# Optimization experiments

Measured on AMD Instinct MI355X. Metric: run time of the kernel, lower is better.

The kernel has to match this reference:

```python
import jax, jax.numpy as jnp
import numpy as np

H_IMG, W_IMG = 60, 80          # hardcoded grid in get_positional_encodings
NUM_HEADS = 8
DIM = 256
N_TOK = H_IMG * W_IMG          # 4800

# Hardcoded intrinsics in the source: fx=517/9, fy=517/8, cx=40, cy=30.
# fx_norm = fx/(2*cx)*2, fy_norm = fy/(2*cy)*2 ; cx_norm = cy_norm = 0,
# so Kinv is diagonal and Kinv @ [x, y, 1] = [x/fx_n, y/fy_n, 1].
_FX_N = (517.0 / 9.0) / 80.0 * 2.0
_FY_N = (517.0 / 8.0) / 60.0 * 2.0


def _positional(B):
    ys = jnp.linspace(-1.0, 1.0, H_IMG)
    xs = jnp.linspace(-1.0, 1.0, W_IMG)
    # loop index j*w + k: y varies over rows (outer), x over cols (inner)
    p3 = jnp.repeat(ys, W_IMG) / _FY_N   # (N,) = y'/w'
    p4 = jnp.tile(xs, H_IMG) / _FX_N     # (N,) = x'/w'
    pos = jnp.stack([p3 * p3, p4 * p4, p3 * p4, p3, p4, jnp.ones_like(p3)], axis=-1)  # (N,6)
    return jnp.broadcast_to(pos, (B, N_TOK, 6))


def setup_inputs() -> dict:
    key = jax.random.key(0)
    k1, k2, k3, k4, k5 = jax.random.split(key, 5)
    B, N, C, H = 1, N_TOK, DIM, NUM_HEADS
    return {
        "x1": jax.random.normal(k1, (B, N, C), dtype=jnp.float32),
        "x2": jax.random.normal(k2, (B, N, C), dtype=jnp.float32),
        "qkv_w": jax.random.normal(k3, (3 * C, C), dtype=jnp.float32) * 0.02,
        "proj_w": jax.random.normal(k4, (C, C + 6 * H), dtype=jnp.float32) * 0.02,
        "proj_b": jax.random.normal(k5, (C,), dtype=jnp.float32) * 0.02,
    }


def reference(x1, x2, qkv_w, proj_w, proj_b):
    B, N, C = x1.shape
    H = NUM_HEADS
    hd = C // H
    scale = hd ** -0.5
    D = hd + 6

    def qkv(x):
        y = (x @ qkv_w.T).reshape(B, N, 3, H, hd).transpose(2, 0, 3, 1, 4)
        return y[0], y[1], y[2]   # each (B,H,N,hd)

    q1, k1, v1 = qkv(x1)
    q2, k2, v2 = qkv(x2)

    pos_h = jnp.broadcast_to(_positional(B)[:, None], (B, H, N, 6))

    def fundamental(q, k, v):
        a = jnp.einsum('bhnd,bhmd->bhnm', q, k) * scale          # (B,H,N,N)
        af = jax.nn.softmax(a, axis=-1) * jax.nn.softmax(a, axis=-2)  # dual softmax
        vc = jnp.concatenate([v, pos_h], axis=-1)                 # (B,H,N,D)
        f = jnp.einsum('bhnc,bhnm->bhcm', vc, af)                 # V^T A
        f = jnp.einsum('bhcm,bhmd->bhcd', f, vc)                  # (V^T A) V -> (B,H,D,D)
        f = f.reshape(B, H * D, D).transpose(0, 2, 1)             # (B, D, H*D)
        return f @ proj_w.T + proj_b                              # (B, D, C)

    fundamental_1 = fundamental(q2, k1, v1)
    fundamental_2 = fundamental(q1, k2, v2)
    return fundamental_2, fundamental_1
```

## Files before the change

### kernel.cpp

```cpp
#include <hip/hip_runtime.h>
#include <stdint.h>
#include <math.h>

#define N_TOK 4800
#define NH 8
#define HD 32
#define DP 40
#define DD 38
#define NTILES 150
#define MCHUNK 3
#define FRAG 2048
#define SCALE 0.17677669529663687f
#define QSCALE (0.17677669529663687f * 1.4426950408889634f)

typedef float f32x16 __attribute__((ext_vector_type(16)));
typedef short s8v __attribute__((ext_vector_type(8)));
typedef int i2v __attribute__((ext_vector_type(2)));

#if __has_builtin(__builtin_amdgcn_exp2f)
#define EXP2F(x) __builtin_amdgcn_exp2f(x)
#else
#define EXP2F(x) exp2f(x)
#endif

__device__ __forceinline__ unsigned short f2bf(float x) {
    union { float f; uint32_t u; } v; v.f = x;
    uint32_t r = v.u + 0x7FFFu + ((v.u >> 16) & 1u);
    return (unsigned short)(r >> 16);
}
__device__ __forceinline__ float bf2f(unsigned short h) {
    union { uint32_t u; float f; } v; v.u = ((uint32_t)h) << 16;
    return v.f;
}
__device__ __forceinline__ int cvtpk(float lo, float hi) {
    int r;
    asm("v_cvt_pk_bf16_f32 %0, %1, %2" : "=v"(r) : "v"(lo), "v"(hi));
    return r;
}
__device__ __forceinline__ s8v mk_s8(int a, int b, int c, int d) {
    union { int i[4]; s8v s; } u;
    u.i[0] = a; u.i[1] = b; u.i[2] = c; u.i[3] = d;
    return u.s;
}

template<int NX, int NY>
__device__ __forceinline__ void swzdec(int& x, int& y, int& z) {
    const int L = blockIdx.x + NX * (blockIdx.y + NY * blockIdx.z);
    constexpr int cpx = NX * NY * 16 / 8;
    const int s = (L & 7) * cpx + (L >> 3);
    x = s % NX;
    const int r = s / NX;
    y = r % NY;
    z = r / NY;
}

#define MFMA(a, b, c) __builtin_amdgcn_mfma_f32_32x32x16_bf16((a), (b), (c), 0, 0, 0)

__global__ __launch_bounds__(256) void frag_kernel(
    const float* __restrict__ x1, unsigned short* __restrict__ xh1,
    unsigned short* __restrict__ xl1,
    const float* __restrict__ x2, unsigned short* __restrict__ xh2,
    unsigned short* __restrict__ xl2,
    const float* __restrict__ w, unsigned short* __restrict__ wh,
    unsigned short* __restrict__ wl)
{
    int b = blockIdx.x;
    const float* src; unsigned short* dh; unsigned short* dl;
    if (b < 150)      { src = x1 + b * 8192; dh = xh1 + b * 8192; dl = xl1 + b * 8192; }
    else if (b < 300) { b -= 150; src = x2 + b * 8192; dh = xh2 + b * 8192; dl = xl2 + b * 8192; }
    else              { b -= 300; src = w + b * 8192; dh = wh + b * 8192; dl = wl + b * 8192; }
    const int t = threadIdx.x;
#pragma unroll
    for (int k = 0; k < 4; ++k) {
        const int f = k * 256 + t;
        const int c = f >> 6;
        const int rem = f & 63;
        const int hi5 = rem >> 5, lr = rem & 31;
        const float* sp = src + lr * 256 + c * 16 + hi5 * 8;
        const float4 a = *(const float4*)(sp);
        const float4 bb = *(const float4*)(sp + 4);
        const float vv[8] = {a.x, a.y, a.z, a.w, bb.x, bb.y, bb.z, bb.w};
        union { unsigned short s[8]; s8v v; } H, L;
#pragma unroll
        for (int j = 0; j < 8; ++j) {
            H.s[j] = f2bf(vv[j]);
            L.s[j] = f2bf(vv[j] - bf2f(H.s[j]));
        }
        *(s8v*)(dh + f * 8) = H.v;
        *(s8v*)(dl + f * 8) = L.v;
    }
}

__global__ __launch_bounds__(128) void qkv_mfma_kernel(
    const unsigned short* __restrict__ xhA, const unsigned short* __restrict__ xlA,
    unsigned short* __restrict__ qbA, unsigned short* __restrict__ kbA,
    float* __restrict__ vcbA,
    const unsigned short* __restrict__ xhB, const unsigned short* __restrict__ xlB,
    unsigned short* __restrict__ qbB, unsigned short* __restrict__ kbB,
    float* __restrict__ vcbB,
    const unsigned short* __restrict__ wh, const unsigned short* __restrict__ wl)
{
    const int sel = blockIdx.z;
    const unsigned short* xh = sel ? xhB : xhA;
    const unsigned short* xl = sel ? xlB : xlA;
    unsigned short* qb = sel ? qbB : qbA;
    unsigned short* kb = sel ? kbB : kbA;
    float* vcb = sel ? vcbB : vcbA;
    const int lane = threadIdx.x & 63;
    const int wid = threadIdx.x >> 6;
    const int xtile = blockIdx.x * 2 + wid;
    const int n0 = xtile * 32;
    const int j0 = blockIdx.y * 32;
    const int lr = lane & 31, hi5 = lane >> 5;
    const unsigned short* xhp = xh + (size_t)xtile * 8192 + lane * 8;
    const unsigned short* xlp = xl + (size_t)xtile * 8192 + lane * 8;
    const unsigned short* whp = wh + (size_t)blockIdx.y * 8192 + lane * 8;
    const unsigned short* wlp = wl + (size_t)blockIdx.y * 8192 + lane * 8;
    f32x16 acc = {};
#pragma unroll 4
    for (int c = 0; c < 16; ++c) {
        const s8v aH = *(const s8v*)(xhp + c * 512);
        const s8v aL = *(const s8v*)(xlp + c * 512);
        const s8v bH = *(const s8v*)(whp + c * 512);
        const s8v bL = *(const s8v*)(wlp + c * 512);
        acc = MFMA(aH, bH, acc);
        acc = MFMA(aH, bL, acc);
        acc = MFMA(aL, bH, acc);
    }
    const int s = j0 >> 8, h = (j0 >> 5) & 7, d = lr;
#pragma unroll
    for (int r = 0; r < 16; ++r) {
        const int n = n0 + (r & 3) + 8 * (r >> 2) + 4 * hi5;
        const float v = acc[r];
        if (s == 2)      vcb[(h * N_TOK + n) * DP + d] = v;
        else if (s == 0) qb[(h * N_TOK + n) * HD + d] = f2bf(v * QSCALE);
        else             kb[(h * N_TOK + n) * HD + d] = f2bf(v);
    }
}

__global__ void pos_kernel(float* __restrict__ vc1, float* __restrict__ vc2)
{
    const int n = blockIdx.x * 256 + threadIdx.x;
    if (n >= N_TOK) return;
    const int row = n / 80, col = n % 80;
    const float y = -1.0f + 2.0f * (float)row / 59.0f;
    const float x = -1.0f + 2.0f * (float)col / 79.0f;
    const float p3 = y * (240.0f / 517.0f);
    const float p4 = x * (360.0f / 517.0f);
    const float pv[8] = {p3 * p3, p4 * p4, p3 * p4, p3, p4, 1.0f, 0.0f, 0.0f};
#pragma unroll
    for (int h = 0; h < NH; ++h) {
        const size_t base = (size_t)(h * N_TOK + n) * DP + 32;
#pragma unroll
        for (int p = 0; p < 8; ++p) {
            vc1[base + p] = pv[p];
            vc2[base + p] = pv[p];
        }
    }
}

__global__ __launch_bounds__(128) void cs_kernel(
    const unsigned short* __restrict__ qbA, const unsigned short* __restrict__ kbA,
    float* __restrict__ csA,
    const unsigned short* __restrict__ qbB, const unsigned short* __restrict__ kbB,
    float* __restrict__ csB)
{
    int bx, by, bz;
    swzdec<75, 5>(bx, by, bz);
    const int sel = bz >> 3;
    const unsigned short* qb = sel ? qbB : qbA;
    const unsigned short* kb = sel ? kbB : kbA;
    float* cs = sel ? csB : csA;
    const int lane = threadIdx.x & 63;
    const int wid = threadIdx.x >> 6;
    const int h = bz & 7;
    const int m0 = bx * 64 + wid * 32;
    const int lr = lane & 31, hi5 = lane >> 5;
    const int hbase = h * N_TOK;
    const unsigned short* kp = kb + (hbase + m0 + lr) * HD + 8 * hi5;
    const s8v bK0 = *(const s8v*)(kp);
    const s8v bK1 = *(const s8v*)(kp + 16);
    const int nt0 = by * 30;
    const unsigned short* qp = qb + (hbase + nt0 * 32 + lr) * HD + 8 * hi5;
    s8v a0 = *(const s8v*)(qp);
    s8v a1 = *(const s8v*)(qp + 16);
    float csa = 0.f, csb = 0.f;
#pragma unroll 2
    for (int it = 0; it < 30; ++it) {
        const int adv = (it < 29) ? (32 * HD) : 0;
        const unsigned short* qpn = qp + adv;
        const s8v na0 = *(const s8v*)(qpn);
        const s8v na1 = *(const s8v*)(qpn + 16);
        f32x16 acc = {};
        acc = MFMA(a0, bK0, acc);
        acc = MFMA(a1, bK1, acc);
#pragma unroll
        for (int r = 0; r < 16; r += 2) {
            csa += EXP2F(acc[r]);
            csb += EXP2F(acc[r + 1]);
        }
        a0 = na0; a1 = na1; qp = qpn;
    }
    float csacc = csa + csb;
    csacc += __shfl_xor(csacc, 32);
    if (lane < 32) atomicAdd(&cs[hbase + m0 + lane], csacc);
}

__global__ __launch_bounds__(256) void vfrag_kernel(
    const float* __restrict__ vcA, const float* __restrict__ csA,
    unsigned short* __restrict__ vfA,
    const float* __restrict__ vcB, const float* __restrict__ csB,
    unsigned short* __restrict__ vfB)
{
    const int sel = blockIdx.y >> 3;
    const float* vc = sel ? vcB : vcA;
    const float* cs = sel ? csB : csA;
    unsigned short* vf = sel ? vfB : vfA;
    __shared__ float vl[32][41];
    __shared__ float ul[32];
    const int mt = blockIdx.x;
    const int h = blockIdx.y & 7;
    const int t = threadIdx.x;
    const int m0 = mt * 32;
    const float* vcbase = vc + (size_t)(h * N_TOK + m0) * DP;
    for (int e = t; e < 32 * DP; e += 256) vl[e / DP][e % DP] = vcbase[e];
    if (t < 32) ul[t] = 1.0f / cs[(size_t)h * N_TOK + m0 + t];
    __syncthreads();
    const int b = t >> 6, lane = t & 63;
    const int hi5 = lane >> 5, lr = lane & 31;
    const int d = (b >> 1) * 32 + lr;
    const int mb = (b & 1) * 16 + hi5 * 8;
    union { unsigned short s[8]; s8v v; } pk;
#pragma unroll
    for (int j = 0; j < 8; ++j) {
        const int mo = mb + j;
        const float v = (d < DP) ? vl[mo][d] * ul[mo] : 0.0f;
        pk.s[j] = f2bf(v);
    }
    *(s8v*)(vf + ((size_t)(h * NTILES + mt) * 4 + b) * 512 + lane * 8) = pk.v;
}

__global__ __launch_bounds__(128, 3) void tprime_mfma_kernel(
    const unsigned short* __restrict__ qbA, const unsigned short* __restrict__ kbA,
    const unsigned short* __restrict__ vfA, float* __restrict__ rsA,
    float* __restrict__ TA0, float* __restrict__ TA1, float* __restrict__ TA2,
    const unsigned short* __restrict__ qbB, const unsigned short* __restrict__ kbB,
    const unsigned short* __restrict__ vfB, float* __restrict__ rsB,
    float* __restrict__ TB0, float* __restrict__ TB1, float* __restrict__ TB2)
{
    int bx, by, bz;
    swzdec<75, MCHUNK>(bx, by, bz);
    const int sel = bz >> 3;
    const unsigned short* qb = sel ? qbB : qbA;
    const unsigned short* kb = sel ? kbB : kbA;
    const unsigned short* vf = sel ? vfB : vfA;
    float* rs = sel ? rsB : rsA;
    float* T = sel ? (by == 0 ? TB0 : (by == 1 ? TB1 : TB2))
                   : (by == 0 ? TA0 : (by == 1 ? TA1 : TA2));
    const int lane = threadIdx.x & 63;
    const int wid = threadIdx.x >> 6;
    const int h = bz & 7;
    const int n0 = bx * 64 + wid * 32;
    const int lr = lane & 31, hi5 = lane >> 5;
    const int hbase = h * N_TOK;
    const unsigned short* qp = qb + (hbase + n0 + lr) * HD + 8 * hi5;
    const s8v bQ0 = *(const s8v*)(qp);
    const s8v bQ1 = *(const s8v*)(qp + 16);
    f32x16 t0 = {}, t1 = {};
    float rsa = 0.f, rsb = 0.f;
    const int mt0 = by * 50;
    const unsigned short* kp = kb + (hbase + mt0 * 32 + lr) * HD + 8 * hi5;
    const unsigned short* vp = vf + ((size_t)(h * NTILES) + mt0) * FRAG + lane * 8;
    s8v a0 = *(const s8v*)(kp);
    s8v a1 = *(const s8v*)(kp + 16);
    s8v v00 = *(const s8v*)(vp);
    s8v v01 = *(const s8v*)(vp + 512);
    s8v v10 = *(const s8v*)(vp + 1024);
    s8v v11 = *(const s8v*)(vp + 1536);
#pragma unroll 2
    for (int it = 0; it < 50; ++it) {
        const int adv = (it < 49) ? 1 : 0;
        const unsigned short* kpn = kp + adv * 32 * HD;
        const unsigned short* vpn = vp + adv * FRAG;
        const s8v na0 = *(const s8v*)(kpn);
        const s8v na1 = *(const s8v*)(kpn + 16);
        const s8v nv00 = *(const s8v*)(vpn);
        const s8v nv01 = *(const s8v*)(vpn + 512);
        const s8v nv10 = *(const s8v*)(vpn + 1024);
        const s8v nv11 = *(const s8v*)(vpn + 1536);
        f32x16 s = {};
        s = MFMA(a0, bQ0, s);
        s = MFMA(a1, bQ1, s);
        float p[16];
#pragma unroll
        for (int r = 0; r < 16; r += 2) {
            const float e0 = EXP2F(s[r]);
            const float e1 = EXP2F(s[r + 1]);
            rsa += e0; rsb += e1;
            p[r] = e0 * e0; p[r + 1] = e1 * e1;
        }
        const int L0 = cvtpk(p[0], p[1]),   L1 = cvtpk(p[2], p[3]);
        const int H0 = cvtpk(p[4], p[5]),   H1 = cvtpk(p[6], p[7]);
        const int L2 = cvtpk(p[8], p[9]),   L3 = cvtpk(p[10], p[11]);
        const int H2 = cvtpk(p[12], p[13]), H3 = cvtpk(p[14], p[15]);
        const i2v s0 = __builtin_amdgcn_permlane32_swap(L0, H0, false, false);
        const i2v s1 = __builtin_amdgcn_permlane32_swap(L1, H1, false, false);
        const i2v s2 = __builtin_amdgcn_permlane32_swap(L2, H2, false, false);
        const i2v s3 = __builtin_amdgcn_permlane32_swap(L3, H3, false, false);
        const s8v pa0 = mk_s8(s0[0], s1[0], s0[1], s1[1]);
        const s8v pa1 = mk_s8(s2[0], s3[0], s2[1], s3[1]);
        __builtin_amdgcn_s_setprio(1);
        t0 = MFMA(pa0, v00, t0);
        t0 = MFMA(pa1, v01, t0);
        t1 = MFMA(pa0, v10, t1);
        t1 = MFMA(pa1, v11, t1);
        __builtin_amdgcn_s_setprio(0);
        a0 = na0; a1 = na1; kp = kpn;
        v00 = nv00; v01 = nv01; v10 = nv10; v11 = nv11; vp = vpn;
    }
    float rsacc = rsa + rsb;
    rsacc += __shfl_xor(rsacc, 32);
    if (lane < 32) atomicAdd(&rs[hbase + n0 + lane], rsacc);
#pragma unroll
    for (int r = 0; r < 16; ++r) {
        const int n = n0 + (r & 3) + 8 * (r >> 2) + 4 * hi5;
        T[(size_t)(hbase + n) * DP + lr] = t0[r];
    }
    if (lr < 8) {
#pragma unroll
        for (int r = 0; r < 16; ++r) {
            const int n = n0 + (r & 3) + 8 * (r >> 2) + 4 * hi5;
            T[(size_t)(hbase + n) * DP + 32 + lr] = t1[r];
        }
    }
}

__global__ __launch_bounds__(256) void fgemm_kernel(
    const float* __restrict__ VCA, const float* __restrict__ rsA,
    const float* __restrict__ TA0, const float* __restrict__ TA1,
    const float* __restrict__ TA2, float* __restrict__ fA,
    const float* __restrict__ VCB, const float* __restrict__ rsB,
    const float* __restrict__ TB0, const float* __restrict__ TB1,
    const float* __restrict__ TB2, float* __restrict__ fB)
{
    const int sel = blockIdx.x >> 3;
    const float* VC = sel ? VCB : VCA;
    const float* rs = sel ? rsB : rsA;
    const float* Ta = sel ? TB0 : TA0;
    const float* Tb = sel ? TB1 : TA1;
    const float* Tc = sel ? TB2 : TA2;
    float* f = sel ? fB : fA;
    __shared__ __align__(16) float wvcl[64 * DP];
    __shared__ __align__(16) float tl[64 * DP];
    __shared__ float wl[64];
    const int h = blockIdx.x & 7, n0 = blockIdx.y * 64;
    const int t = threadIdx.x;
    if (t < 64) wl[t] = 1.0f / rs[(size_t)h * N_TOK + n0 + t];
    __syncthreads();
    const float* vcbase = VC + (size_t)(h * N_TOK + n0) * DP;
    const float* tabase = Ta + (size_t)(h * N_TOK + n0) * DP;
    const float* tbbase = Tb + (size_t)(h * N_TOK + n0) * DP;
    const float* tcbase = Tc + (size_t)(h * N_TOK + n0) * DP;
    for (int e = t; e < 64 * DP; e += 256) {
        wvcl[e] = vcbase[e] * wl[e / DP];
        tl[e] = tabase[e] + tbbase[e] + tcbase[e];
    }
    __syncthreads();
    for (int p = t; p < DD * DD; p += 256) {
        const int c = p / DD, d = p % DD;
        float s = 0.f;
#pragma unroll 8
        for (int n = 0; n < 64; ++n) s += wvcl[n * DP + c] * tl[n * DP + d];
        atomicAdd(&f[(size_t)(h * DD + c) * DP + d], s);
    }
}

__global__ __launch_bounds__(256) void out_kernel(
    const float* __restrict__ f1, const float* __restrict__ f2,
    const float* __restrict__ pw, const float* __restrict__ pb,
    float* __restrict__ out)
{
    const int sel = blockIdx.y;
    const float* f = sel ? f2 : f1;
    float* dst = sel ? out : (out + DD * 256);
    __shared__ __align__(16) float flds[304];
    const int d = blockIdx.x, t = threadIdx.x;
    for (int j = t; j < 304; j += 256) flds[j] = f[(size_t)j * DP + d];
    __syncthreads();
    float acc = pb[t];
    const float* pwrow = pw + (size_t)t * 304;
#pragma unroll 4
    for (int j = 0; j < 304; j += 4) {
        const float4 p4 = *(const float4*)&pwrow[j];
        const float4 f4 = *(const float4*)&flds[j];
        acc += p4.x * f4.x + p4.y * f4.y + p4.z * f4.z + p4.w * f4.w;
    }
    dst[(size_t)d * 256 + t] = acc;
}

extern "C" void kernel_launch(void* const* d_in, const int* in_sizes, int n_in,
                              void* d_out, int out_size, void* d_ws, size_t ws_size,
                              hipStream_t stream)
{
    const float* x1 = (const float*)d_in[0];
    const float* x2 = (const float*)d_in[1];
    const float* qkv_w = (const float*)d_in[2];
    const float* proj_w = (const float*)d_in[3];
    const float* proj_b = (const float*)d_in[4];
    float* out = (float*)d_out;

    const size_t QSZ = (size_t)NH * N_TOK * HD;
    const size_t VSZ = (size_t)NH * N_TOK * DP;
    const size_t SSZ = (size_t)NH * N_TOK;
    const size_t FSZ = (size_t)NH * DD * DP;
    const size_t XSZ = (size_t)N_TOK * 256;
    const size_t WSZ = (size_t)768 * 256;
    const size_t VTSZ = (size_t)NH * NTILES * FRAG;

    float* vc1 = (float*)d_ws;
    float* vc2 = vc1 + VSZ;
    float* rs1 = vc2 + VSZ;
    float* cs1 = rs1 + SSZ;
    float* rs2 = cs1 + SSZ;
    float* cs2 = rs2 + SSZ;
    float* f1 = cs2 + SSZ;
    float* f2 = f1 + FSZ;
    float* T1a = f2 + FSZ;
    float* T1b = T1a + VSZ;
    float* T1c = T1b + VSZ;
    float* T2a = T1c + VSZ;
    float* T2b = T2a + VSZ;
    float* T2c = T2b + VSZ;
    unsigned short* xh1 = (unsigned short*)(T2c + VSZ);
    unsigned short* xl1 = xh1 + XSZ;
    unsigned short* xh2 = xl1 + XSZ;
    unsigned short* xl2 = xh2 + XSZ;
    unsigned short* wh = xl2 + XSZ;
    unsigned short* wl = wh + WSZ;
    unsigned short* qb1 = wl + WSZ;
    unsigned short* kb1 = qb1 + QSZ;
    unsigned short* qb2 = kb1 + QSZ;
    unsigned short* kb2 = qb2 + QSZ;
    unsigned short* vf1 = kb2 + QSZ;
    unsigned short* vf2 = vf1 + VTSZ;

    const size_t zbytes = (4 * SSZ + 2 * FSZ) * sizeof(float);
    hipMemsetAsync(rs1, 0, zbytes, stream);

    frag_kernel<<<324, 256, 0, stream>>>(x1, xh1, xl1, x2, xh2, xl2,
                                         qkv_w, wh, wl);

    qkv_mfma_kernel<<<dim3(75, 24, 2), 128, 0, stream>>>(
        xh1, xl1, qb1, kb1, vc1, xh2, xl2, qb2, kb2, vc2, wh, wl);
    pos_kernel<<<19, 256, 0, stream>>>(vc1, vc2);

    cs_kernel<<<dim3(75, 5, 16), 128, 0, stream>>>(qb2, kb1, cs1,
                                                   qb1, kb2, cs2);
    vfrag_kernel<<<dim3(150, 16), 256, 0, stream>>>(vc1, cs1, vf1,
                                                    vc2, cs2, vf2);
    tprime_mfma_kernel<<<dim3(75, MCHUNK, 16), 128, 0, stream>>>(
        qb2, kb1, vf1, rs1, T1a, T1b, T1c,
        qb1, kb2, vf2, rs2, T2a, T2b, T2c);
    fgemm_kernel<<<dim3(16, 75), 256, 0, stream>>>(
        vc1, rs1, T1a, T1b, T1c, f1,
        vc2, rs2, T2a, T2b, T2c, f2);
    out_kernel<<<dim3(38, 2), 256, 0, stream>>>(f1, f2, proj_w, proj_b, out);
}
```

Baseline: 244.3 us.

## Drop split-bf16 QKV, compute positional features inline, widen attention blocks

Result: faster. 230.4 us (-5.7%).

```diff
diff --git a/kernel.cpp b/kernel.cpp
--- a/kernel.cpp
+++ b/kernel.cpp
@@ -28,10 +28,6 @@
     uint32_t r = v.u + 0x7FFFu + ((v.u >> 16) & 1u);
     return (unsigned short)(r >> 16);
 }
-__device__ __forceinline__ float bf2f(unsigned short h) {
-    union { uint32_t u; float f; } v; v.u = ((uint32_t)h) << 16;
-    return v.f;
-}
 __device__ __forceinline__ int cvtpk(float lo, float hi) {
     int r;
     asm("v_cvt_pk_bf16_f32 %0, %1, %2" : "=v"(r) : "v"(lo), "v"(hi));
@@ -42,11 +38,24 @@
     u.i[0] = a; u.i[1] = b; u.i[2] = c; u.i[3] = d;
     return u.s;
 }
-
-template<int NX, int NY>
+__device__ __forceinline__ float posv(int m, int idx) {
+    const int rrow = m / 80, rcol = m % 80;
+    const float y = -1.0f + (float)rrow * (2.0f / 59.0f);
+    const float x = -1.0f + (float)rcol * (2.0f / 79.0f);
+    const float p3 = y * (240.0f / 517.0f);
+    const float p4 = x * (360.0f / 517.0f);
+    if (idx == 0) return p3 * p3;
+    if (idx == 1) return p4 * p4;
+    if (idx == 2) return p3 * p4;
+    if (idx == 3) return p3;
+    if (idx == 4) return p4;
+    return 1.0f;
+}
+
+template<int NX, int NY, int NZ>
 __device__ __forceinline__ void swzdec(int& x, int& y, int& z) {
     const int L = blockIdx.x + NX * (blockIdx.y + NY * blockIdx.z);
-    constexpr int cpx = NX * NY * 16 / 8;
+    constexpr int cpx = NX * NY * NZ / 8;
     const int s = (L & 7) * cpx + (L >> 3);
     x = s % NX;
     const int r = s / NX;
@@ -58,115 +67,93 @@
 
 __global__ __launch_bounds__(256) void frag_kernel(
     const float* __restrict__ x1, unsigned short* __restrict__ xh1,
-    unsigned short* __restrict__ xl1,
     const float* __restrict__ x2, unsigned short* __restrict__ xh2,
-    unsigned short* __restrict__ xl2,
-    const float* __restrict__ w, unsigned short* __restrict__ wh,
-    unsigned short* __restrict__ wl)
+    const float* __restrict__ w, unsigned short* __restrict__ wh)
 {
     int b = blockIdx.x;
-    const float* src; unsigned short* dh; unsigned short* dl;
-    if (b < 150)      { src = x1 + b * 8192; dh = xh1 + b * 8192; dl = xl1 + b * 8192; }
-    else if (b < 300) { b -= 150; src = x2 + b * 8192; dh = xh2 + b * 8192; dl = xl2 + b * 8192; }
-    else              { b -= 300; src = w + b * 8192; dh = wh + b * 8192; dl = wl + b * 8192; }
+    const float* src; unsigned short* dh;
+    if (b < 150)      { src = x1 + b * 8192; dh = xh1 + b * 8192; }
+    else if (b < 300) { b -= 150; src = x2 + b * 8192; dh = xh2 + b * 8192; }
+    else              { b -= 300; src = w + b * 8192; dh = wh + b * 8192; }
     const int t = threadIdx.x;
 #pragma unroll
     for (int k = 0; k < 4; ++k) {
         const int f = k * 256 + t;
         const int c = f >> 6;
         const int rem = f & 63;
-        const int hi5 = rem >> 5, lr = rem & 31;
-        const float* sp = src + lr * 256 + c * 16 + hi5 * 8;
+        const float* sp = src + (rem & 31) * 256 + c * 16 + (rem >> 5) * 8;
         const float4 a = *(const float4*)(sp);
         const float4 bb = *(const float4*)(sp + 4);
         const float vv[8] = {a.x, a.y, a.z, a.w, bb.x, bb.y, bb.z, bb.w};
-        union { unsigned short s[8]; s8v v; } H, L;
-#pragma unroll
-        for (int j = 0; j < 8; ++j) {
-            H.s[j] = f2bf(vv[j]);
-            L.s[j] = f2bf(vv[j] - bf2f(H.s[j]));
-        }
+        union { unsigned short s[8]; s8v v; } H;
+#pragma unroll
+        for (int j = 0; j < 8; ++j) H.s[j] = f2bf(vv[j]);
         *(s8v*)(dh + f * 8) = H.v;
-        *(s8v*)(dl + f * 8) = L.v;
-    }
-}
-
-__global__ __launch_bounds__(128) void qkv_mfma_kernel(
-    const unsigned short* __restrict__ xhA, const unsigned short* __restrict__ xlA,
-    unsigned short* __restrict__ qbA, unsigned short* __restrict__ kbA,
-    float* __restrict__ vcbA,
-    const unsigned short* __restrict__ xhB, const unsigned short* __restrict__ xlB,
-    unsigned short* __restrict__ qbB, unsigned short* __restrict__ kbB,
-    float* __restrict__ vcbB,
-    const unsigned short* __restrict__ wh, const unsigned short* __restrict__ wl)
-{
-    const int sel = blockIdx.z;
+    }
+}
+
+__global__ __launch_bounds__(128, 4) void qkv_mfma_kernel(
+    const unsigned short* __restrict__ xhA, unsigned short* __restrict__ qbA,
+    unsigned short* __restrict__ kbA, float* __restrict__ vcbA,
+    const unsigned short* __restrict__ xhB, unsigned short* __restrict__ qbB,
+    unsigned short* __restrict__ kbB, float* __restrict__ vcbB,
+    const unsigned short* __restrict__ wh)
+{
+    int bx, by, bz;
+    swzdec<75, 12, 2>(bx, by, bz);
+    const int sel = bz;
     const unsigned short* xh = sel ? xhB : xhA;
-    const unsigned short* xl = sel ? xlB : xlA;
     unsigned short* qb = sel ? qbB : qbA;
     unsigned short* kb = sel ? kbB : kbA;
     float* vcb = sel ? vcbB : vcbA;
     const int lane = threadIdx.x & 63;
     const int wid = threadIdx.x >> 6;
-    const int xtile = blockIdx.x * 2 + wid;
-    const int n0 = xtile * 32;
-    const int j0 = blockIdx.y * 32;
+    const int xtile = bx * 2 + wid;
+    const unsigned short* xp = xh + (size_t)xtile * 8192 + lane * 8;
+    const unsigned short* wp0 = wh + (size_t)(by * 2) * 8192 + lane * 8;
+    const unsigned short* wp1 = wp0 + 8192;
+    f32x16 acc0 = {}, acc1 = {};
+#pragma unroll
+    for (int c = 0; c < 16; ++c) {
+        const s8v aH = *(const s8v*)(xp + c * 512);
+        const s8v b0 = *(const s8v*)(wp0 + c * 512);
+        const s8v b1 = *(const s8v*)(wp1 + c * 512);
+        acc0 = MFMA(aH, b0, acc0);
+        acc1 = MFMA(aH, b1, acc1);
+    }
     const int lr = lane & 31, hi5 = lane >> 5;
-    const unsigned short* xhp = xh + (size_t)xtile * 8192 + lane * 8;
-    const unsigned short* xlp = xl + (size_t)xtile * 8192 + lane * 8;
-    const unsigned short* whp = wh + (size_t)blockIdx.y * 8192 + lane * 8;
-    const unsigned short* wlp = wl + (size_t)blockIdx.y * 8192 + lane * 8;
-    f32x16 acc = {};
-#pragma unroll 4
-    for (int c = 0; c < 16; ++c) {
-        const s8v aH = *(const s8v*)(xhp + c * 512);
-        const s8v aL = *(const s8v*)(xlp + c * 512);
-        const s8v bH = *(const s8v*)(whp + c * 512);
-        const s8v bL = *(const s8v*)(wlp + c * 512);
-        acc = MFMA(aH, bH, acc);
-        acc = MFMA(aH, bL, acc);
-        acc = MFMA(aL, bH, acc);
-    }
-    const int s = j0 >> 8, h = (j0 >> 5) & 7, d = lr;
-#pragma unroll
-    for (int r = 0; r < 16; ++r) {
-        const int n = n0 + (r & 3) + 8 * (r >> 2) + 4 * hi5;
-        const float v = acc[r];
-        if (s == 2)      vcb[(h * N_TOK + n) * DP + d] = v;
-        else if (s == 0) qb[(h * N_TOK + n) * HD + d] = f2bf(v * QSCALE);
-        else             kb[(h * N_TOK + n) * HD + d] = f2bf(v);
-    }
-}
-
-__global__ void pos_kernel(float* __restrict__ vc1, float* __restrict__ vc2)
-{
-    const int n = blockIdx.x * 256 + threadIdx.x;
-    if (n >= N_TOK) return;
-    const int row = n / 80, col = n % 80;
-    const float y = -1.0f + 2.0f * (float)row / 59.0f;
-    const float x = -1.0f + 2.0f * (float)col / 79.0f;
-    const float p3 = y * (240.0f / 517.0f);
-    const float p4 = x * (360.0f / 517.0f);
-    const float pv[8] = {p3 * p3, p4 * p4, p3 * p4, p3, p4, 1.0f, 0.0f, 0.0f};
-#pragma unroll
-    for (int h = 0; h < NH; ++h) {
-        const size_t base = (size_t)(h * N_TOK + n) * DP + 32;
-#pragma unroll
-        for (int p = 0; p < 8; ++p) {
-            vc1[base + p] = pv[p];
-            vc2[base + p] = pv[p];
+    {
+        const int jt = by * 2, s = jt >> 3, h = jt & 7;
+#pragma unroll
+        for (int r = 0; r < 16; ++r) {
+            const int n = xtile * 32 + (r & 3) + 8 * (r >> 2) + 4 * hi5;
+            const float v = acc0[r];
+            if (s == 2)      vcb[(h * N_TOK + n) * HD + lr] = v;
+            else if (s == 0) qb[(h * N_TOK + n) * HD + lr] = f2bf(v * QSCALE);
+            else             kb[(h * N_TOK + n) * HD + lr] = f2bf(v);
         }
     }
-}
-
-__global__ __launch_bounds__(128) void cs_kernel(
+    {
+        const int jt = by * 2 + 1, s = jt >> 3, h = jt & 7;
+#pragma unroll
+        for (int r = 0; r < 16; ++r) {
+            const int n = xtile * 32 + (r & 3) + 8 * (r >> 2) + 4 * hi5;
+            const float v = acc1[r];
+            if (s == 2)      vcb[(h * N_TOK + n) * HD + lr] = v;
+            else if (s == 0) qb[(h * N_TOK + n) * HD + lr] = f2bf(v * QSCALE);
+            else             kb[(h * N_TOK + n) * HD + lr] = f2bf(v);
+        }
+    }
+}
+
+__global__ __launch_bounds__(192, 4) void cs_kernel(
     const unsigned short* __restrict__ qbA, const unsigned short* __restrict__ kbA,
     float* __restrict__ csA,
     const unsigned short* __restrict__ qbB, const unsigned short* __restrict__ kbB,
     float* __restrict__ csB)
 {
     int bx, by, bz;
-    swzdec<75, 5>(bx, by, bz);
+    swzdec<50, 5, 16>(bx, by, bz);
     const int sel = bz >> 3;
     const unsigned short* qb = sel ? qbB : qbA;
     const unsigned short* kb = sel ? kbB : kbA;
@@ -174,23 +161,21 @@
     const int lane = threadIdx.x & 63;
     const int wid = threadIdx.x >> 6;
     const int h = bz & 7;
-    const int m0 = bx * 64 + wid * 32;
+    const int m0 = bx * 96 + wid * 32;
     const int lr = lane & 31, hi5 = lane >> 5;
     const int hbase = h * N_TOK;
     const unsigned short* kp = kb + (hbase + m0 + lr) * HD + 8 * hi5;
     const s8v bK0 = *(const s8v*)(kp);
     const s8v bK1 = *(const s8v*)(kp + 16);
-    const int nt0 = by * 30;
-    const unsigned short* qp = qb + (hbase + nt0 * 32 + lr) * HD + 8 * hi5;
+    const unsigned short* qp = qb + (hbase + by * 960 + lr) * HD + 8 * hi5;
     s8v a0 = *(const s8v*)(qp);
     s8v a1 = *(const s8v*)(qp + 16);
     float csa = 0.f, csb = 0.f;
 #pragma unroll 2
     for (int it = 0; it < 30; ++it) {
-        const int adv = (it < 29) ? (32 * HD) : 0;
-        const unsigned short* qpn = qp + adv;
-        const s8v na0 = *(const s8v*)(qpn);
-        const s8v na1 = *(const s8v*)(qpn + 16);
+        qp += 32 * HD;
+        const s8v na0 = *(const s8v*)(qp);
+        const s8v na1 = *(const s8v*)(qp + 16);
         f32x16 acc = {};
         acc = MFMA(a0, bK0, acc);
         acc = MFMA(a1, bK1, acc);
@@ -199,7 +184,7 @@
             csa += EXP2F(acc[r]);
             csb += EXP2F(acc[r + 1]);
         }
-        a0 = na0; a1 = na1; qp = qpn;
+        a0 = na0; a1 = na1;
     }
     float csacc = csa + csb;
     csacc += __shfl_xor(csacc, 32);
@@ -216,14 +201,14 @@
     const float* vc = sel ? vcB : vcA;
     const float* cs = sel ? csB : csA;
     unsigned short* vf = sel ? vfB : vfA;
-    __shared__ float vl[32][41];
+    __shared__ float vl[32][33];
     __shared__ float ul[32];
     const int mt = blockIdx.x;
     const int h = blockIdx.y & 7;
     const int t = threadIdx.x;
     const int m0 = mt * 32;
-    const float* vcbase = vc + (size_t)(h * N_TOK + m0) * DP;
-    for (int e = t; e < 32 * DP; e += 256) vl[e / DP][e % DP] = vcbase[e];
+    const float* vcbase = vc + (size_t)(h * N_TOK + m0) * HD;
+    for (int e = t; e < 32 * HD; e += 256) vl[e >> 5][e & 31] = vcbase[e];
     if (t < 32) ul[t] = 1.0f / cs[(size_t)h * N_TOK + m0 + t];
     __syncthreads();
     const int b = t >> 6, lane = t & 63;
@@ -234,13 +219,16 @@
 #pragma unroll
     for (int j = 0; j < 8; ++j) {
         const int mo = mb + j;
-        const float v = (d < DP) ? vl[mo][d] * ul[mo] : 0.0f;
-        pk.s[j] = f2bf(v);
+        float v;
+        if (d < 32)      v = vl[mo][d];
+        else if (d < 38) v = posv(m0 + mo, d - 32);
+        else             v = 0.0f;
+        pk.s[j] = f2bf(v * ul[mo]);
     }
     *(s8v*)(vf + ((size_t)(h * NTILES + mt) * 4 + b) * 512 + lane * 8) = pk.v;
 }
 
-__global__ __launch_bounds__(128, 3) void tprime_mfma_kernel(
+__global__ __launch_bounds__(192, 4) void tprime_mfma_kernel(
     const unsigned short* __restrict__ qbA, const unsigned short* __restrict__ kbA,
     const unsigned short* __restrict__ vfA, float* __restrict__ rsA,
     float* __restrict__ TA0, float* __restrict__ TA1, float* __restrict__ TA2,
@@ -249,7 +237,7 @@
     float* __restrict__ TB0, float* __restrict__ TB1, float* __restrict__ TB2)
 {
     int bx, by, bz;
-    swzdec<75, MCHUNK>(bx, by, bz);
+    swzdec<50, MCHUNK, 16>(bx, by, bz);
     const int sel = bz >> 3;
     const unsigned short* qb = sel ? qbB : qbA;
     const unsigned short* kb = sel ? kbB : kbA;
@@ -260,7 +248,7 @@
     const int lane = threadIdx.x & 63;
     const int wid = threadIdx.x >> 6;
     const int h = bz & 7;
-    const int n0 = bx * 64 + wid * 32;
+    const int n0 = bx * 96 + wid * 32;
     const int lr = lane & 31, hi5 = lane >> 5;
     const int hbase = h * N_TOK;
     const unsigned short* qp = qb + (hbase + n0 + lr) * HD + 8 * hi5;
@@ -270,7 +258,7 @@
     float rsa = 0.f, rsb = 0.f;
     const int mt0 = by * 50;
     const unsigned short* kp = kb + (hbase + mt0 * 32 + lr) * HD + 8 * hi5;
-    const unsigned short* vp = vf + ((size_t)(h * NTILES) + mt0) * FRAG + lane * 8;
+    const unsigned short* vp = vf + (size_t)(h * NTILES + mt0) * FRAG + lane * 8;
     s8v a0 = *(const s8v*)(kp);
     s8v a1 = *(const s8v*)(kp + 16);
     s8v v00 = *(const s8v*)(vp);
@@ -279,15 +267,13 @@
     s8v v11 = *(const s8v*)(vp + 1536);
 #pragma unroll 2
     for (int it = 0; it < 50; ++it) {
-        const int adv = (it < 49) ? 1 : 0;
-        const unsigned short* kpn = kp + adv * 32 * HD;
-        const unsigned short* vpn = vp + adv * FRAG;
-        const s8v na0 = *(const s8v*)(kpn);
-        const s8v na1 = *(const s8v*)(kpn + 16);
-        const s8v nv00 = *(const s8v*)(vpn);
-        const s8v nv01 = *(const s8v*)(vpn + 512);
-        const s8v nv10 = *(const s8v*)(vpn + 1024);
-        const s8v nv11 = *(const s8v*)(vpn + 1536);
+        kp += 32 * HD; vp += FRAG;
+        const s8v na0 = *(const s8v*)(kp);
+        const s8v na1 = *(const s8v*)(kp + 16);
+        const s8v nv00 = *(const s8v*)(vp);
+        const s8v nv01 = *(const s8v*)(vp + 512);
+        const s8v nv10 = *(const s8v*)(vp + 1024);
+        const s8v nv11 = *(const s8v*)(vp + 1536);
         f32x16 s = {};
         s = MFMA(a0, bQ0, s);
         s = MFMA(a1, bQ1, s);
@@ -315,8 +301,8 @@
         t1 = MFMA(pa0, v10, t1);
         t1 = MFMA(pa1, v11, t1);
         __builtin_amdgcn_s_setprio(0);
-        a0 = na0; a1 = na1; kp = kpn;
-        v00 = nv00; v01 = nv01; v10 = nv10; v11 = nv11; vp = vpn;
+        a0 = na0; a1 = na1;
+        v00 = nv00; v01 = nv01; v10 = nv10; v11 = nv11;
     }
     float rsacc = rsa + rsb;
     rsacc += __shfl_xor(rsacc, 32);
@@ -357,12 +343,17 @@
     const int t = threadIdx.x;
     if (t < 64) wl[t] = 1.0f / rs[(size_t)h * N_TOK + n0 + t];
     __syncthreads();
-    const float* vcbase = VC + (size_t)(h * N_TOK + n0) * DP;
+    const float* vcbase = VC + (size_t)(h * N_TOK + n0) * HD;
     const float* tabase = Ta + (size_t)(h * N_TOK + n0) * DP;
     const float* tbbase = Tb + (size_t)(h * N_TOK + n0) * DP;
     const float* tcbase = Tc + (size_t)(h * N_TOK + n0) * DP;
     for (int e = t; e < 64 * DP; e += 256) {
-        wvcl[e] = vcbase[e] * wl[e / DP];
+        const int row = e / DP, c = e - row * DP;
+        float v;
+        if (c < 32)      v = vcbase[row * HD + c];
+        else if (c < 38) v = posv(n0 + row, c - 32);
+        else             v = 0.0f;
+        wvcl[e] = v * wl[row];
         tl[e] = tabase[e] + tbbase[e] + tcbase[e];
     }
     __syncthreads();
@@ -418,8 +409,8 @@
     const size_t VTSZ = (size_t)NH * NTILES * FRAG;
 
     float* vc1 = (float*)d_ws;
-    float* vc2 = vc1 + VSZ;
-    float* rs1 = vc2 + VSZ;
+    float* vc2 = vc1 + QSZ;
+    float* rs1 = vc2 + QSZ;
     float* cs1 = rs1 + SSZ;
     float* rs2 = cs1 + SSZ;
     float* cs2 = rs2 + SSZ;
@@ -432,12 +423,9 @@
     float* T2b = T2a + VSZ;
     float* T2c = T2b + VSZ;
     unsigned short* xh1 = (unsigned short*)(T2c + VSZ);
-    unsigned short* xl1 = xh1 + XSZ;
-    unsigned short* xh2 = xl1 + XSZ;
-    unsigned short* xl2 = xh2 + XSZ;
-    unsigned short* wh = xl2 + XSZ;
-    unsigned short* wl = wh + WSZ;
-    unsigned short* qb1 = wl + WSZ;
+    unsigned short* xh2 = xh1 + XSZ;
+    unsigned short* wh = xh2 + XSZ;
+    unsigned short* qb1 = wh + WSZ;
     unsigned short* kb1 = qb1 + QSZ;
     unsigned short* qb2 = kb1 + QSZ;
     unsigned short* kb2 = qb2 + QSZ;
@@ -447,18 +435,16 @@
     const size_t zbytes = (4 * SSZ + 2 * FSZ) * sizeof(float);
     hipMemsetAsync(rs1, 0, zbytes, stream);
 
-    frag_kernel<<<324, 256, 0, stream>>>(x1, xh1, xl1, x2, xh2, xl2,
-                                         qkv_w, wh, wl);
-
-    qkv_mfma_kernel<<<dim3(75, 24, 2), 128, 0, stream>>>(
-        xh1, xl1, qb1, kb1, vc1, xh2, xl2, qb2, kb2, vc2, wh, wl);
-    pos_kernel<<<19, 256, 0, stream>>>(vc1, vc2);
-
-    cs_kernel<<<dim3(75, 5, 16), 128, 0, stream>>>(qb2, kb1, cs1,
+    frag_kernel<<<324, 256, 0, stream>>>(x1, xh1, x2, xh2, qkv_w, wh);
+
+    qkv_mfma_kernel<<<dim3(75, 12, 2), 128, 0, stream>>>(
+        xh1, qb1, kb1, vc1, xh2, qb2, kb2, vc2, wh);
+
+    cs_kernel<<<dim3(50, 5, 16), 192, 0, stream>>>(qb2, kb1, cs1,
                                                    qb1, kb2, cs2);
     vfrag_kernel<<<dim3(150, 16), 256, 0, stream>>>(vc1, cs1, vf1,
                                                     vc2, cs2, vf2);
-    tprime_mfma_kernel<<<dim3(75, MCHUNK, 16), 128, 0, stream>>>(
+    tprime_mfma_kernel<<<dim3(50, MCHUNK, 16), 192, 0, stream>>>(
         qb2, kb1, vf1, rs1, T1a, T1b, T1c,
         qb1, kb2, vf2, rs2, T2a, T2b, T2c);
     fgemm_kernel<<<dim3(16, 75), 256, 0, stream>>>(
```
